# Performance work log

Measured on AMD Instinct MI355X. Metric: run time of the kernel, lower is better.

The kernel has to match this reference:

```python
import math
import jax, jax.numpy as jnp
import numpy as np

D_MODEL, D_HEAD, N_HEADS, COND = 1024, 64, 16, 1024
BATCH, L_T, H_S, W_S = 2, 8, 16, 16
N_FREQS = D_HEAD // 8  # rotary freqs per axis; 3 axes -> rotates 3*D_HEAD/4 dims
EPS = 1e-6


def _ste(x, qx):
    # straight-through estimator: forward qx, backward identity
    return x + jax.lax.stop_gradient(qx - x)


def _weight_quant(w):
    # BitNet-1.58 ternary: per-tensor absmean scale, round to {-1,0,1}
    s = 1.0 / jnp.clip(jnp.mean(jnp.abs(w)), 1e-5)
    return jnp.clip(jnp.round(w * s), -1.0, 1.0) / s


def _act_quant(x):
    # per-token int8 absmax quant
    s = 127.0 / jnp.clip(jnp.max(jnp.abs(x), axis=-1, keepdims=True), 1e-5)
    return jnp.clip(jnp.round(x * s), -128.0, 127.0) / s


def bit_linear(x, w):
    return _ste(x, _act_quant(x)) @ _ste(w, _weight_quant(w)).T


def rms_norm(x, scale, eps=EPS):
    ms = jnp.mean(x * x, axis=-1, keepdims=True)
    return x * scale * jax.lax.rsqrt(ms + eps)


def apply_rotary_emb(x, theta):
    # rotate first 2*d dims of x (d = theta.shape[-1]); pass the rest through
    d = theta.shape[-1]
    x1, x2, x3 = x[..., :d], x[..., d:2 * d], x[..., 2 * d:]
    cos, sin = jnp.cos(theta), jnp.sin(theta)
    return jnp.concatenate([x1 * cos - x2 * sin, x2 * cos + x1 * sin, x3], axis=-1)


def make_freqs():
    # log-spaced pi..10*pi, distributed across heads (k-diffusion AxialRoPE init)
    log_min, log_max = math.log(math.pi), math.log(10.0 * math.pi)
    f = jnp.exp(jnp.linspace(log_min, log_max, N_HEADS * N_FREQS + 1)[:-1])
    return f.reshape(N_FREQS, N_HEADS).T.astype(jnp.float32)  # [n_heads, n_freqs]


def setup_inputs() -> dict:
    key = jax.random.key(0)
    ks = jax.random.split(key, 6)
    x = jax.random.normal(ks[0], (BATCH, L_T, H_S, W_S, D_MODEL), jnp.float32)
    pos = jax.random.uniform(ks[1], (BATCH, L_T, H_S, W_S, 3), jnp.float32) * 2.0 - 1.0
    cond = jax.random.normal(ks[2], (BATCH, COND), jnp.float32)
    norm_w = jax.random.normal(ks[3], (D_MODEL, COND), jnp.float32) * 0.02
    qkv_w = jax.random.normal(ks[4], (3 * D_MODEL, D_MODEL), jnp.float32) * 0.02
    out_w = jax.random.normal(ks[5], (D_MODEL, D_MODEL), jnp.float32) * 0.02
    scale = jnp.full((N_HEADS,), 10.0, jnp.float32)
    freqs = make_freqs()
    return dict(x=x, pos=pos, cond=cond, norm_w=norm_w, qkv_w=qkv_w,
                out_w=out_w, scale=scale, freqs=freqs)


def reference(x, pos, cond, norm_w, qkv_w, out_w, scale, freqs):
    n, l, h, w, d = x.shape
    L = l * h * w
    skip = x
    # AdaRMSNorm: scale = 1 + zero-init Linear(cond)
    ada = 1.0 + cond @ norm_w.T                      # [n, d]
    xn = rms_norm(x, ada[:, None, None, None, :])
    # BitLinear QKV projection
    qkv = bit_linear(xn.reshape(n, L, d), qkv_w)     # [n, L, 3d]
    qkv = qkv.reshape(n, L, 3, N_HEADS, D_HEAD).transpose(2, 0, 3, 1, 4)  # [3,n,nh,L,e]
    q, k, v = qkv[0], qkv[1], qkv[2]
    # cosine-sim rescale with learned per-head scale
    sqrt_s = jnp.sqrt(scale)[:, None, None]          # [nh,1,1]
    q = q * (sqrt_s * jax.lax.rsqrt(jnp.sum(q * q, -1, keepdims=True) + EPS))
    k = k * (sqrt_s * jax.lax.rsqrt(jnp.sum(k * k, -1, keepdims=True) + EPS))
    # axial RoPE over 3 axes
    p = pos.reshape(n, L, 3)
    theta = jnp.concatenate([p[..., None, a:a + 1] * freqs for a in range(3)], axis=-1)  # [n,L,nh,3*nf]
    theta = jnp.moveaxis(theta, -2, -3)              # [n,nh,L,3*nf]
    q = apply_rotary_emb(q, theta)
    k = apply_rotary_emb(k, theta)
    # SDPA with scale=1.0 (cosine-sim already scaled)
    attn = jax.nn.softmax(jnp.einsum('nhqe,nhke->nhqk', q, k), axis=-1)
    o = jnp.einsum('nhqk,nhke->nhqe', attn, v)       # [n,nh,L,e]
    o = o.transpose(0, 2, 1, 3).reshape(n, L, d)
    o = bit_linear(o, out_w).reshape(n, l, h, w, d)
    return o + skip
```

## Files before the change

kernel.cpp:

```cpp
#include <hip/hip_runtime.h>
#include <hip/hip_bf16.h>
#include <math.h>

typedef __attribute__((ext_vector_type(8))) short bf16x8;
typedef __attribute__((ext_vector_type(4))) short bf16x4;
typedef __attribute__((ext_vector_type(4))) float f32x4;
typedef __attribute__((ext_vector_type(16))) float f32x16;
typedef __attribute__((ext_vector_type(4))) unsigned u32x4;
typedef __attribute__((ext_vector_type(2))) unsigned u32x2;
typedef __attribute__((ext_vector_type(4))) int i32x4;

#define DEV static __device__ __forceinline__
#define LOG2E 1.4426950408889634f

DEV unsigned short f2bf(float f) {
  unsigned int u = __float_as_uint(f);
  u += 0x7FFFu + ((u >> 16) & 1u);
  return (unsigned short)(u >> 16);
}
DEV float bf2f(unsigned short h) { return __uint_as_float(((unsigned int)h) << 16); }
DEV unsigned cvtpk(float lo, float hi) {
  unsigned r;
  asm("v_cvt_pk_bf16_f32 %0, %1, %2" : "=v"(r) : "v"(lo), "v"(hi));
  return r;
}
DEV float exp2raw(float x) {
  float r;
  asm("v_exp_f32 %0, %1" : "=v"(r) : "v"(x));
  return r;
}
DEV float wsum(float v) { for (int o = 32; o; o >>= 1) v += __shfl_xor(v, o); return v; }
DEV float wmaxr(float v) { for (int o = 32; o; o >>= 1) v = fmaxf(v, __shfl_xor(v, o)); return v; }

DEV void gload_lds16(const void* g, void* s) {
  __builtin_amdgcn_global_load_lds(
      (const __attribute__((address_space(1))) unsigned int*)g,
      (__attribute__((address_space(3))) unsigned int*)s, 16, 0, 0);
}

__global__ __launch_bounds__(256) void wred_k(const float* __restrict__ qw,
                                              const float* __restrict__ ow,
                                              float* __restrict__ rowsum) {
  int row = blockIdx.x;
  const float* p = (row < 3072) ? (qw + (size_t)row * 1024)
                                : (ow + (size_t)(row - 3072) * 1024);
  f32x4 v = *(const f32x4*)&p[threadIdx.x * 4];
  float s = fabsf(v[0]) + fabsf(v[1]) + fabsf(v[2]) + fabsf(v[3]);
  s = wsum(s);
  __shared__ float sh[4];
  if ((threadIdx.x & 63) == 0) sh[threadIdx.x >> 6] = s;
  __syncthreads();
  if (threadIdx.x == 0) rowsum[row] = sh[0] + sh[1] + sh[2] + sh[3];
}

__global__ __launch_bounds__(256) void finalize_k(const float* __restrict__ rowsum,
                                                  float* __restrict__ scales) {
  float s1 = 0.f, s2 = 0.f;
  for (int i = threadIdx.x; i < 3072; i += 256) s1 += rowsum[i];
  for (int i = threadIdx.x; i < 1024; i += 256) s2 += rowsum[3072 + i];
  s1 = wsum(s1); s2 = wsum(s2);
  __shared__ float sh1[4], sh2[4];
  if ((threadIdx.x & 63) == 0) { sh1[threadIdx.x >> 6] = s1; sh2[threadIdx.x >> 6] = s2; }
  __syncthreads();
  if (threadIdx.x == 0) {
    float m1 = fmaxf((sh1[0] + sh1[1] + sh1[2] + sh1[3]) / (3072.f * 1024.f), 1e-5f);
    float m2 = fmaxf((sh2[0] + sh2[1] + sh2[2] + sh2[3]) / (1024.f * 1024.f), 1e-5f);
    scales[0] = m1; scales[1] = 1.f / m1;
    scales[2] = m2; scales[3] = 1.f / m2;
  }
}

__global__ __launch_bounds__(256) void wquant_k(const float* __restrict__ qw,
                                                const float* __restrict__ ow,
                                                const float* __restrict__ scales,
                                                signed char* __restrict__ Wq,
                                                signed char* __restrict__ Wo) {
  int i0 = (blockIdx.x * 256 + threadIdx.x) * 4;
  if (i0 < 3072 * 1024) {
    f32x4 v = *(const f32x4*)&qw[i0];
    unsigned pk = 0;
    for (int j = 0; j < 4; j++) {
      int t = (int)fminf(fmaxf(rintf(v[j] * scales[1]), -1.f), 1.f);
      pk |= ((unsigned)t & 0xFFu) << (8 * j);
    }
    *(unsigned*)&Wq[i0] = pk;
  } else {
    int k = i0 - 3072 * 1024;
    f32x4 v = *(const f32x4*)&ow[k];
    unsigned pk = 0;
    for (int j = 0; j < 4; j++) {
      int t = (int)fminf(fmaxf(rintf(v[j] * scales[3]), -1.f), 1.f);
      pk |= ((unsigned)t & 0xFFu) << (8 * j);
    }
    *(unsigned*)&Wo[k] = pk;
  }
}

__global__ __launch_bounds__(256) void ada_k(const float* __restrict__ cond,
                                             const float* __restrict__ nw,
                                             float* __restrict__ ada) {
  int j = blockIdx.x * 4 + (threadIdx.x >> 6);
  int b = blockIdx.y;
  int l = threadIdx.x & 63;
  const float* cp = cond + b * 1024;
  const float* wp = nw + (size_t)j * 1024;
  float s = 0.f;
  for (int c = l; c < 1024; c += 64) s += cp[c] * wp[c];
  s = wsum(s);
  if (l == 0) ada[b * 1024 + j] = 1.f + s;
}

__global__ __launch_bounds__(256) void rmsq_k(const float* __restrict__ x,
                                              const float* __restrict__ ada,
                                              signed char* __restrict__ Aq,
                                              float* __restrict__ ascale) {
  int row = blockIdx.x;
  int b = row >> 11;
  const float* xr = x + (size_t)row * 1024;
  const float* ar = ada + b * 1024;
  int t4 = threadIdx.x * 4;
  f32x4 v = *(const f32x4*)&xr[t4];
  float ss = v[0]*v[0] + v[1]*v[1] + v[2]*v[2] + v[3]*v[3];
  ss = wsum(ss);
  __shared__ float sh[4], sh2[4];
  if ((threadIdx.x & 63) == 0) sh[threadIdx.x >> 6] = ss;
  __syncthreads();
  float inv = rsqrtf((sh[0] + sh[1] + sh[2] + sh[3]) * (1.f / 1024.f) + 1e-6f);
  f32x4 a = *(const f32x4*)&ar[t4];
  float xn[4]; float mx = 0.f;
  for (int i = 0; i < 4; i++) { xn[i] = v[i] * a[i] * inv; mx = fmaxf(mx, fabsf(xn[i])); }
  mx = wmaxr(mx);
  if ((threadIdx.x & 63) == 0) sh2[threadIdx.x >> 6] = mx;
  __syncthreads();
  float rmax = fmaxf(fmaxf(sh2[0], sh2[1]), fmaxf(sh2[2], sh2[3]));
  float s = 127.f / fmaxf(rmax, 1e-5f);
  unsigned pk = 0;
  for (int i = 0; i < 4; i++) {
    int ai = (int)fminf(fmaxf(rintf(xn[i] * s), -128.f), 127.f);
    pk |= ((unsigned)ai & 0xFFu) << (8 * i);
  }
  *(unsigned*)&Aq[(size_t)row * 1024 + t4] = pk;
  if (threadIdx.x == 0) ascale[row] = 1.f / s;
}

__global__ __launch_bounds__(256) void oquant_k(const unsigned short* __restrict__ Opart,
                                                const float* __restrict__ ms,
                                                signed char* __restrict__ Oq,
                                                float* __restrict__ oscale) {
  int row = blockIdx.x;
  int b = row >> 11, qrow = row & 2047;
  int t4 = threadIdx.x * 4;
  int h = t4 >> 6, e0 = t4 & 63;
  int bh = b * 16 + h;
  size_t i0 = (size_t)bh * 2048 + qrow;
  size_t i1 = (size_t)(32 + bh) * 2048 + qrow;
  float w = 1.f / (ms[i0] + ms[i1]);
  bf16x4 o0 = *(const bf16x4*)&Opart[i0 * 64 + e0];
  bf16x4 o1 = *(const bf16x4*)&Opart[i1 * 64 + e0];
  float v[4]; float mx = 0.f;
  for (int i = 0; i < 4; i++) {
    v[i] = (bf2f((unsigned short)o0[i]) + bf2f((unsigned short)o1[i])) * w;
    mx = fmaxf(mx, fabsf(v[i]));
  }
  mx = wmaxr(mx);
  __shared__ float sh[4];
  if ((threadIdx.x & 63) == 0) sh[threadIdx.x >> 6] = mx;
  __syncthreads();
  float rmax = fmaxf(fmaxf(sh[0], sh[1]), fmaxf(sh[2], sh[3]));
  float s = 127.f / fmaxf(rmax, 1e-5f);
  unsigned pk = 0;
  for (int i = 0; i < 4; i++) {
    int ai = (int)fminf(fmaxf(rintf(v[i] * s), -128.f), 127.f);
    pk |= ((unsigned)ai & 0xFFu) << (8 * i);
  }
  *(unsigned*)&Oq[(size_t)row * 1024 + t4] = pk;
  if (threadIdx.x == 0) oscale[row] = 1.f / s;
}

__global__ __launch_bounds__(256, 3) void gemm_i8(const signed char* __restrict__ A8,
                                                  const signed char* __restrict__ B8,
                                                  int N, int K, int nwg, int mode,
                                                  const float* __restrict__ rowsc,
                                                  const float* __restrict__ wscp,
                                                  const float* __restrict__ skip,
                                                  float* __restrict__ outF,
                                                  unsigned short* __restrict__ outB) {
  __shared__ signed char As[128 * 64];
  __shared__ signed char Bs[128 * 64];
  int bid = blockIdx.x;
  int wg = (bid % 8) * (nwg >> 3) + (bid >> 3);
  int bx = wg & 31, by = wg >> 5;
  int tid = threadIdx.x;
  int w = tid >> 6, l = tid & 63;
  int q = l & 15, g = l >> 4;
  int tm = bx * 128, tn = by * 128;
  int wr = w >> 1, wc = w & 1;
  float wsc = wscp[0];
  i32x4 acc[4][4];
  i32x4 zero = {0, 0, 0, 0};
#pragma unroll
  for (int m = 0; m < 4; m++)
#pragma unroll
    for (int n = 0; n < 4; n++) acc[m][n] = zero;
  int s0 = w * 64 + l, s1 = 256 + s0;
  int r0 = s0 >> 2, p0 = s0 & 3, gs0 = p0 ^ ((r0 >> 1) & 3);
  int r1 = s1 >> 2, p1 = s1 & 3, gs1 = p1 ^ ((r1 >> 1) & 3);
  const signed char* Ag0 = A8 + (size_t)(tm + r0) * K + gs0 * 16;
  const signed char* Ag1 = A8 + (size_t)(tm + r1) * K + gs1 * 16;
  const signed char* Bg0 = B8 + (size_t)(tn + r0) * K + gs0 * 16;
  const signed char* Bg1 = B8 + (size_t)(tn + r1) * K + gs1 * 16;
  int posq = ((q >> 1) & 3);
  for (int k0 = 0; k0 < K; k0 += 64) {
    gload_lds16(Ag0 + k0, &As[w * 1024]);
    gload_lds16(Ag1 + k0, &As[4096 + w * 1024]);
    gload_lds16(Bg0 + k0, &Bs[w * 1024]);
    gload_lds16(Bg1 + k0, &Bs[4096 + w * 1024]);
    __syncthreads();
    int pg = (g ^ posq) * 16;
    i32x4 af[4], bfr[4];
#pragma unroll
    for (int m = 0; m < 4; m++)
      af[m] = *(const i32x4*)&As[(wr * 64 + m * 16 + q) * 64 + pg];
#pragma unroll
    for (int n = 0; n < 4; n++)
      bfr[n] = *(const i32x4*)&Bs[(wc * 64 + n * 16 + q) * 64 + pg];
#pragma unroll
    for (int m = 0; m < 4; m++)
#pragma unroll
      for (int n = 0; n < 4; n++)
        acc[m][n] = __builtin_amdgcn_mfma_i32_16x16x64_i8(af[m], bfr[n], acc[m][n], 0, 0, 0);
    __syncthreads();
  }
#pragma unroll
  for (int m = 0; m < 4; m++) {
#pragma unroll
    for (int r = 0; r < 4; r++) {
      int row = tm + wr * 64 + m * 16 + g * 4 + r;
      float dq = rowsc[row] * wsc;
#pragma unroll
      for (int n = 0; n < 4; n++) {
        int col = tn + wc * 64 + n * 16 + q;
        float vv = (float)acc[m][n][r] * dq;
        if (mode == 0) outB[(size_t)row * N + col] = f2bf(vv);
        else { size_t idx = (size_t)row * N + col; outF[idx] = vv + skip[idx]; }
      }
    }
  }
}

__global__ __launch_bounds__(256) void prep_k(const unsigned short* __restrict__ qkv,
                                              const float* __restrict__ pos,
                                              const float* __restrict__ scale,
                                              const float* __restrict__ freqs,
                                              unsigned short* __restrict__ Qo,
                                              unsigned short* __restrict__ Ko,
                                              unsigned short* __restrict__ VT) {
  __shared__ unsigned short tile[64][72];
  int tid = threadIdx.x;
  if (blockIdx.x < 16384) {
    int w = tid >> 6, l = tid & 63;
    int gw = blockIdx.x * 4 + w;
    int h = gw & 15, t = (gw >> 4) & 2047, b = gw >> 15;
    const unsigned short* base = qkv + ((size_t)(b * 2048 + t)) * 3072 + h * 64 + l;
    float qv = bf2f(base[0]);
    float kv = bf2f(base[1024]);
    float sq = qv * qv, sk = kv * kv;
    for (int o = 32; o; o >>= 1) { sq += __shfl_xor(sq, o); sk += __shfl_xor(sk, o); }
    float ssc = sqrtf(scale[h]);
    float fq = ssc * rsqrtf(sq + 1e-6f);
    float fk = ssc * rsqrtf(sk + 1e-6f);
    float qn = qv * fq, kn = kv * fk;
    int e = l;
    int idx24 = (e < 24) ? e : e - 24;
    int partner = (e < 24) ? e + 24 : ((e < 48) ? e - 24 : e);
    float qo = __shfl(qn, partner), ko = __shfl(kn, partner);
    float qr = qn, kr = kn;
    if (e < 48) {
      int a = idx24 >> 3, f = idx24 & 7;
      float th = pos[((size_t)(b * 2048 + t)) * 3 + a] * freqs[h * 8 + f];
      float sn, cs; __sincosf(th, &sn, &cs);
      if (e < 24) { qr = qn * cs - qo * sn; kr = kn * cs - ko * sn; }
      else        { qr = qn * cs + qo * sn; kr = kn * cs + ko * sn; }
    }
    size_t oi = ((size_t)((b * 16 + h) * 2048 + t)) * 64 + e;
    Qo[oi] = f2bf(qr * LOG2E);
    Ko[oi] = f2bf(kr);
  } else {
    int bid2 = blockIdx.x - 16384;
    int tt = bid2 & 31, bh = bid2 >> 5;
    int b = bh >> 4, h = bh & 15;
    for (int ro = 0; ro < 2; ro++) {
      int r = ro * 32 + (tid >> 3);
      int c = (tid & 7) * 8;
      *(bf16x8*)&tile[r][c] =
          *(const bf16x8*)(qkv + ((size_t)(b * 2048 + tt * 64 + r)) * 3072 + 2048 + h * 64 + c);
    }
    __syncthreads();
    int e = tid >> 2;
    int tc = (tid & 3) * 16;
    bf16x8 o0, o1;
#pragma unroll
    for (int i = 0; i < 4; i++) {
      o0[i]     = (short)tile[tc + i][e];
      o0[4 + i] = (short)tile[tc + 8 + i][e];
      o1[i]     = (short)tile[tc + 4 + i][e];
      o1[4 + i] = (short)tile[tc + 12 + i][e];
    }
    unsigned short* dst = VT + ((size_t)(bh * 64 + e)) * 2048 + tt * 64 + tc;
    *(bf16x8*)dst = o0;
    *(bf16x8*)(dst + 8) = o1;
  }
}

__global__ __launch_bounds__(512, 4) void attn_k(const unsigned short* __restrict__ Q,
                                                 const unsigned short* __restrict__ K,
                                                 const unsigned short* __restrict__ VT,
                                                 unsigned short* __restrict__ Opart,
                                                 float* __restrict__ ms) {
  __shared__ unsigned short Ks[2][128 * 64];
  __shared__ unsigned short Vs[2][64 * 128];
  const float M0 = 15.0f;
  int tid = threadIdx.x;
  int w = tid >> 6, l = tid & 63;
  int q = l & 31, hi = l >> 5;
  int bid = blockIdx.x;
  int sbh = (bid >> 6) * 8 + (bid & 7);
  int qg = (bid >> 3) & 7;
  int split = sbh >> 5, bh = sbh & 31;
  int qrow0 = qg * 256 + w * 32;
  const unsigned short* Kbase = K + (size_t)bh * 2048 * 64 + (size_t)split * 1024 * 64;
  const unsigned short* Vbase = VT + (size_t)bh * 64 * 2048 + split * 1024;

  bf16x8 qa[4];
#pragma unroll
  for (int s = 0; s < 4; s++)
    qa[s] = *(const bf16x8*)(Q + ((size_t)bh * 2048 + qrow0 + q) * 64 + s * 16 + hi * 8);

  int koff0[4], koff1[4], voff0[4], voff1[4];
#pragma unroll
  for (int se = 0; se < 4; se++) {
    int gk = se * 2 + hi;
    koff0[se] = q * 64 + ((gk ^ (q & 7)) * 8);
    koff1[se] = (32 + q) * 64 + ((gk ^ (q & 7)) * 8);
    voff0[se] = q * 128 + ((gk ^ (q & 7)) * 8);
    voff1[se] = (32 + q) * 128 + ((gk ^ (q & 7)) * 8);
  }

  int slA = tid, slB = 512 + tid;
  int krA = slA >> 3, kgA = (slA & 7) ^ (krA & 7);
  int krB = slB >> 3, kgB = (slB & 7) ^ (krB & 7);
  int vrA = slA >> 4, vgA = (slA & 15) ^ (vrA & 7);
  int vrB = slB >> 4, vgB = (slB & 15) ^ (vrB & 7);
  const unsigned short* KgA = Kbase + (size_t)krA * 64 + kgA * 8;
  const unsigned short* KgB = Kbase + (size_t)krB * 64 + kgB * 8;
  const unsigned short* VgA = Vbase + (size_t)vrA * 2048 + vgA * 8;
  const unsigned short* VgB = Vbase + (size_t)vrB * 2048 + vgB * 8;

  f32x16 acc0, acc1, fz;
  for (int i = 0; i < 16; i++) { acc0[i] = 0.f; acc1[i] = 0.f; fz[i] = 0.f; }
  float sum = 0.f;

  auto stage = [&](int buf, int kt) {
    gload_lds16(KgA + (size_t)kt * 64, &Ks[buf][(w * 64) * 8]);
    gload_lds16(KgB + (size_t)kt * 64, &Ks[buf][(512 + w * 64) * 8]);
    gload_lds16(VgA + kt, &Vs[buf][(w * 64) * 8]);
    gload_lds16(VgB + kt, &Vs[buf][(512 + w * 64) * 8]);
  };

  stage(0, 0);
  __syncthreads();
  int cur = 0;
  for (int it = 0; it < 8; it++) {
    if (it < 7) stage(cur ^ 1, (it + 1) * 128);
    const unsigned short* Ksc = Ks[cur];
    const unsigned short* Vsc = Vs[cur];
#pragma unroll
    for (int ss = 0; ss < 2; ss++) {
      int kro = ss * 4096;
      int vco = ss * 64;
      bf16x8 ka0 = *(const bf16x8*)&Ksc[kro + koff0[0]];
      bf16x8 ka1 = *(const bf16x8*)&Ksc[kro + koff1[0]];
      __builtin_amdgcn_s_setprio(1);
      f32x16 s0 = __builtin_amdgcn_mfma_f32_32x32x16_bf16(ka0, qa[0], fz, 0, 0, 0);
      f32x16 s1 = __builtin_amdgcn_mfma_f32_32x32x16_bf16(ka1, qa[0], fz, 0, 0, 0);
#pragma unroll
      for (int se = 1; se < 4; se++) {
        ka0 = *(const bf16x8*)&Ksc[kro + koff0[se]];
        ka1 = *(const bf16x8*)&Ksc[kro + koff1[se]];
        s0 = __builtin_amdgcn_mfma_f32_32x32x16_bf16(ka0, qa[se], s0, 0, 0, 0);
        s1 = __builtin_amdgcn_mfma_f32_32x32x16_bf16(ka1, qa[se], s1, 0, 0, 0);
      }
      __builtin_amdgcn_s_setprio(0);

      bf16x8 pf[4];
#pragma unroll
      for (int n = 0; n < 4; n++) {
        int o = (n & 1) * 8;
        u32x4 t;
#pragma unroll
        for (int j = 0; j < 4; j++) {
          float a = (n < 2) ? s0[o + 2 * j] : s1[o + 2 * j];
          float b = (n < 2) ? s0[o + 2 * j + 1] : s1[o + 2 * j + 1];
          float e0 = exp2raw(a - M0);
          float e1 = exp2raw(b - M0);
          sum += e0 + e1;
          t[j] = cvtpk(e0, e1);
        }
        pf[n] = __builtin_bit_cast(bf16x8, t);
      }

      __builtin_amdgcn_s_setprio(1);
#pragma unroll
      for (int n = 0; n < 4; n++) {
        bf16x8 va0 = *(const bf16x8*)&Vsc[vco + voff0[n]];
        bf16x8 va1 = *(const bf16x8*)&Vsc[vco + voff1[n]];
        acc0 = __builtin_amdgcn_mfma_f32_32x32x16_bf16(va0, pf[n], acc0, 0, 0, 0);
        acc1 = __builtin_amdgcn_mfma_f32_32x32x16_bf16(va1, pf[n], acc1, 0, 0, 0);
      }
      __builtin_amdgcn_s_setprio(0);
    }
    __syncthreads();
    cur ^= 1;
  }

  sum += __shfl_xor(sum, 32);
  size_t prow = (size_t)(split * 32 + bh) * 2048 + qrow0 + q;
  unsigned short* Op = Opart + prow * 64;
#pragma unroll
  for (int et = 0; et < 2; et++) {
    const f32x16& a = et ? acc1 : acc0;
#pragma unroll
    for (int qd = 0; qd < 4; qd++) {
      int e0 = et * 32 + 4 * hi + qd * 8;
      u32x2 t;
      t[0] = cvtpk(a[qd * 4 + 0], a[qd * 4 + 1]);
      t[1] = cvtpk(a[qd * 4 + 2], a[qd * 4 + 3]);
      *(bf16x4*)&Op[e0] = __builtin_bit_cast(bf16x4, t);
    }
  }
  if (hi == 0) ms[prow] = sum;
}

extern "C" void kernel_launch(void* const* d_in, const int* in_sizes, int n_in,
                              void* d_out, int out_size, void* d_ws, size_t ws_size,
                              hipStream_t stream) {
  const float* x      = (const float*)d_in[0];
  const float* pos    = (const float*)d_in[1];
  const float* cond   = (const float*)d_in[2];
  const float* norm_w = (const float*)d_in[3];
  const float* qkv_w  = (const float*)d_in[4];
  const float* out_w  = (const float*)d_in[5];
  const float* scale  = (const float*)d_in[6];
  const float* freqs  = (const float*)d_in[7];
  float* out = (float*)d_out;
  char* ws = (char*)d_ws;

  const size_t o_ada    = 0;
  const size_t o_rowsum = 8192;
  const size_t o_scales = 24576;
  const size_t o_ascale = 24832;
  const size_t o_oscale = 41216;
  const size_t o_Wq8    = 57600;
  const size_t o_Wo8    = o_Wq8 + 3145728;
  const size_t o_AqQ    = o_Wo8 + 1048576;
  const size_t o_qkv    = o_AqQ + 8388608;
  const size_t o_K      = o_qkv + 25165824;
  const size_t o_VT     = o_K + 8388608;

  float* ada            = (float*)(ws + o_ada);
  float* rowsum         = (float*)(ws + o_rowsum);
  float* scales         = (float*)(ws + o_scales);
  float* ascale         = (float*)(ws + o_ascale);
  float* oscale         = (float*)(ws + o_oscale);
  signed char* Wq8      = (signed char*)(ws + o_Wq8);
  signed char* Wo8      = (signed char*)(ws + o_Wo8);
  signed char* Aq8      = (signed char*)(ws + o_AqQ);
  unsigned short* Qb    = (unsigned short*)(ws + o_AqQ);
  unsigned short* qkv   = (unsigned short*)(ws + o_qkv);
  unsigned short* Opart = (unsigned short*)(ws + o_qkv);
  float* msb            = (float*)(ws + o_qkv + 2ull*32*2048*64*2);
  unsigned short* Kb    = (unsigned short*)(ws + o_K);
  signed char* Oq8      = (signed char*)(ws + o_K);
  unsigned short* VT    = (unsigned short*)(ws + o_VT);

  wred_k<<<4096, 256, 0, stream>>>(qkv_w, out_w, rowsum);
  finalize_k<<<1, 256, 0, stream>>>(rowsum, scales);
  wquant_k<<<4096, 256, 0, stream>>>(qkv_w, out_w, scales, Wq8, Wo8);
  ada_k<<<dim3(256, 2), 256, 0, stream>>>(cond, norm_w, ada);
  rmsq_k<<<4096, 256, 0, stream>>>(x, ada, Aq8, ascale);
  gemm_i8<<<768, 256, 0, stream>>>(Aq8, Wq8, 3072, 1024, 768, 0, ascale, &scales[0],
                                   nullptr, nullptr, qkv);
  prep_k<<<17408, 256, 0, stream>>>(qkv, pos, scale, freqs, Qb, Kb, VT);
  attn_k<<<512, 512, 0, stream>>>(Qb, Kb, VT, Opart, msb);
  oquant_k<<<4096, 256, 0, stream>>>(Opart, msb, Oq8, oscale);
  gemm_i8<<<256, 256, 0, stream>>>(Oq8, Wo8, 1024, 1024, 256, 1, oscale, &scales[2],
                                   x, out, nullptr);
}
```

Measured before the change: 150.1 us.

## Double-buffer int8 GEMM LDS, fuse weight-quant with ada, use hardware sin/cos

The int8 GEMM now keeps two LDS buffers and issues the global-to-LDS load for the next K tile before computing the current one, so load latency can overlap the MFMAs. This doubles LDS use per block, which may lower occupancy at the requested three blocks per CU. The weight-quant and ada-projection kernels are merged into one launch to save a launch. RoPE sin/cos now use raw v_sin/v_cos on the fraction of theta/2π, which is cheaper but slightly less accurate.

New measurement: 149.4 us, median of 2. About the same (-0.5%).

```diff
diff --git a/kernel.cpp b/kernel.cpp
--- a/kernel.cpp
+++ b/kernel.cpp
@@ -12,6 +12,7 @@
 
 #define DEV static __device__ __forceinline__
 #define LOG2E 1.4426950408889634f
+#define INV2PI 0.15915494309189535f
 
 DEV unsigned short f2bf(float f) {
   unsigned int u = __float_as_uint(f);
@@ -29,6 +30,9 @@
   asm("v_exp_f32 %0, %1" : "=v"(r) : "v"(x));
   return r;
 }
+DEV float fract_raw(float x) { float r; asm("v_fract_f32 %0, %1" : "=v"(r) : "v"(x)); return r; }
+DEV float sin_rev(float x)   { float r; asm("v_sin_f32 %0, %1"   : "=v"(r) : "v"(x)); return r; }
+DEV float cos_rev(float x)   { float r; asm("v_cos_f32 %0, %1"   : "=v"(r) : "v"(x)); return r; }
 DEV float wsum(float v) { for (int o = 32; o; o >>= 1) v += __shfl_xor(v, o); return v; }
 DEV float wmaxr(float v) { for (int o = 32; o; o >>= 1) v = fmaxf(v, __shfl_xor(v, o)); return v; }
 
@@ -70,44 +74,46 @@
   }
 }
 
-__global__ __launch_bounds__(256) void wquant_k(const float* __restrict__ qw,
-                                                const float* __restrict__ ow,
-                                                const float* __restrict__ scales,
-                                                signed char* __restrict__ Wq,
-                                                signed char* __restrict__ Wo) {
-  int i0 = (blockIdx.x * 256 + threadIdx.x) * 4;
-  if (i0 < 3072 * 1024) {
-    f32x4 v = *(const f32x4*)&qw[i0];
-    unsigned pk = 0;
-    for (int j = 0; j < 4; j++) {
-      int t = (int)fminf(fmaxf(rintf(v[j] * scales[1]), -1.f), 1.f);
-      pk |= ((unsigned)t & 0xFFu) << (8 * j);
-    }
-    *(unsigned*)&Wq[i0] = pk;
+__global__ __launch_bounds__(256) void wqada_k(const float* __restrict__ qw,
+                                               const float* __restrict__ ow,
+                                               const float* __restrict__ scales,
+                                               const float* __restrict__ cond,
+                                               const float* __restrict__ nw,
+                                               signed char* __restrict__ Wq,
+                                               signed char* __restrict__ Wo,
+                                               float* __restrict__ ada) {
+  if (blockIdx.x < 4096) {
+    int i0 = (blockIdx.x * 256 + threadIdx.x) * 4;
+    if (i0 < 3072 * 1024) {
+      f32x4 v = *(const f32x4*)&qw[i0];
+      unsigned pk = 0;
+      for (int j = 0; j < 4; j++) {
+        int t = (int)fminf(fmaxf(rintf(v[j] * scales[1]), -1.f), 1.f);
+        pk |= ((unsigned)t & 0xFFu) << (8 * j);
+      }
+      *(unsigned*)&Wq[i0] = pk;
+    } else {
+      int k = i0 - 3072 * 1024;
+      f32x4 v = *(const f32x4*)&ow[k];
+      unsigned pk = 0;
+      for (int j = 0; j < 4; j++) {
+        int t = (int)fminf(fmaxf(rintf(v[j] * scales[3]), -1.f), 1.f);
+        pk |= ((unsigned)t & 0xFFu) << (8 * j);
+      }
+      *(unsigned*)&Wo[k] = pk;
+    }
   } else {
-    int k = i0 - 3072 * 1024;
-    f32x4 v = *(const f32x4*)&ow[k];
-    unsigned pk = 0;
-    for (int j = 0; j < 4; j++) {
-      int t = (int)fminf(fmaxf(rintf(v[j] * scales[3]), -1.f), 1.f);
-      pk |= ((unsigned)t & 0xFFu) << (8 * j);
-    }
-    *(unsigned*)&Wo[k] = pk;
-  }
-}
-
-__global__ __launch_bounds__(256) void ada_k(const float* __restrict__ cond,
-                                             const float* __restrict__ nw,
-                                             float* __restrict__ ada) {
-  int j = blockIdx.x * 4 + (threadIdx.x >> 6);
-  int b = blockIdx.y;
-  int l = threadIdx.x & 63;
-  const float* cp = cond + b * 1024;
-  const float* wp = nw + (size_t)j * 1024;
-  float s = 0.f;
-  for (int c = l; c < 1024; c += 64) s += cp[c] * wp[c];
-  s = wsum(s);
-  if (l == 0) ada[b * 1024 + j] = 1.f + s;
+    int bid2 = blockIdx.x - 4096;
+    int b = bid2 >> 8;
+    int j = (bid2 & 255) * 4 + (threadIdx.x >> 6);
+    int l = threadIdx.x & 63;
+    const float* cp = cond + b * 1024;
+    const float* wp = nw + (size_t)j * 1024;
+    float s = 0.f;
+    for (int c = l; c < 1024; c += 64) s += cp[c] * wp[c];
+    s = wsum(s);
+    if (l == 0) ada[b * 1024 + j] = 1.f + s;
+  }
 }
 
 __global__ __launch_bounds__(256) void rmsq_k(const float* __restrict__ x,
@@ -185,8 +191,8 @@
                                                   const float* __restrict__ skip,
                                                   float* __restrict__ outF,
                                                   unsigned short* __restrict__ outB) {
-  __shared__ signed char As[128 * 64];
-  __shared__ signed char Bs[128 * 64];
+  __shared__ signed char As[2][128 * 64];
+  __shared__ signed char Bs[2][128 * 64];
   int bid = blockIdx.x;
   int wg = (bid % 8) * (nwg >> 3) + (bid >> 3);
   int bx = wg & 31, by = wg >> 5;
@@ -210,26 +216,34 @@
   const signed char* Bg0 = B8 + (size_t)(tn + r0) * K + gs0 * 16;
   const signed char* Bg1 = B8 + (size_t)(tn + r1) * K + gs1 * 16;
   int posq = ((q >> 1) & 3);
+
+  auto stage = [&](int buf, int k0) {
+    gload_lds16(Ag0 + k0, &As[buf][w * 1024]);
+    gload_lds16(Ag1 + k0, &As[buf][4096 + w * 1024]);
+    gload_lds16(Bg0 + k0, &Bs[buf][w * 1024]);
+    gload_lds16(Bg1 + k0, &Bs[buf][4096 + w * 1024]);
+  };
+
+  stage(0, 0);
+  __syncthreads();
+  int cur = 0;
   for (int k0 = 0; k0 < K; k0 += 64) {
-    gload_lds16(Ag0 + k0, &As[w * 1024]);
-    gload_lds16(Ag1 + k0, &As[4096 + w * 1024]);
-    gload_lds16(Bg0 + k0, &Bs[w * 1024]);
-    gload_lds16(Bg1 + k0, &Bs[4096 + w * 1024]);
-    __syncthreads();
+    if (k0 + 64 < K) stage(cur ^ 1, k0 + 64);
     int pg = (g ^ posq) * 16;
     i32x4 af[4], bfr[4];
 #pragma unroll
     for (int m = 0; m < 4; m++)
-      af[m] = *(const i32x4*)&As[(wr * 64 + m * 16 + q) * 64 + pg];
+      af[m] = *(const i32x4*)&As[cur][(wr * 64 + m * 16 + q) * 64 + pg];
 #pragma unroll
     for (int n = 0; n < 4; n++)
-      bfr[n] = *(const i32x4*)&Bs[(wc * 64 + n * 16 + q) * 64 + pg];
+      bfr[n] = *(const i32x4*)&Bs[cur][(wc * 64 + n * 16 + q) * 64 + pg];
 #pragma unroll
     for (int m = 0; m < 4; m++)
 #pragma unroll
       for (int n = 0; n < 4; n++)
         acc[m][n] = __builtin_amdgcn_mfma_i32_16x16x64_i8(af[m], bfr[n], acc[m][n], 0, 0, 0);
     __syncthreads();
+    cur ^= 1;
   }
 #pragma unroll
   for (int m = 0; m < 4; m++) {
@@ -278,7 +292,8 @@
     if (e < 48) {
       int a = idx24 >> 3, f = idx24 & 7;
       float th = pos[((size_t)(b * 2048 + t)) * 3 + a] * freqs[h * 8 + f];
-      float sn, cs; __sincosf(th, &sn, &cs);
+      float rev = fract_raw(th * INV2PI);
+      float sn = sin_rev(rev), cs = cos_rev(rev);
       if (e < 24) { qr = qn * cs - qo * sn; kr = kn * cs - ko * sn; }
       else        { qr = qn * cs + qo * sn; kr = kn * cs + ko * sn; }
     }
@@ -485,8 +500,7 @@
 
   wred_k<<<4096, 256, 0, stream>>>(qkv_w, out_w, rowsum);
   finalize_k<<<1, 256, 0, stream>>>(rowsum, scales);
-  wquant_k<<<4096, 256, 0, stream>>>(qkv_w, out_w, scales, Wq8, Wo8);
-  ada_k<<<dim3(256, 2), 256, 0, stream>>>(cond, norm_w, ada);
+  wqada_k<<<4608, 256, 0, stream>>>(qkv_w, out_w, scales, cond, norm_w, Wq8, Wo8, ada);
   rmsq_k<<<4096, 256, 0, stream>>>(x, ada, Aq8, ascale);
   gemm_i8<<<768, 256, 0, stream>>>(Aq8, Wq8, 3072, 1024, 768, 0, ascale, &scales[0],
                                    nullptr, nullptr, qkv);
```
